# Optimization experiments

Hardware: AMD Instinct MI355X
Metric: run time of the kernel (lower is better)

Reference implementation:

```python
import jax, jax.numpy as jnp
import numpy as np

B, T, H = 4, 8192, 512
LN_EPS = 1e-5


def _ln(x, g, b):
    mu = jnp.mean(x, axis=-1, keepdims=True)
    var = jnp.mean((x - mu) ** 2, axis=-1, keepdims=True)
    return (x - mu) * jax.lax.rsqrt(var + LN_EPS) * g + b


def _log_g(x):
    # log of g(x) = x + 0.5 (x >= 0) else sigmoid(x); both branches NaN-safe.
    return jnp.where(x >= 0, jnp.log(jax.nn.relu(x) + 0.5), -jax.nn.softplus(-x))


def _min_gru(x, Wz, bz, Wh, bh):
    # minGRU parallel log-space scan ("Were RNNs All We Needed?" Alg.), h_0 = 0.
    k = x @ Wz + bz                      # [B,T,H] gate pre-activation
    log_z = -jax.nn.softplus(-k)         # log sigmoid(k)
    log_coeffs = -jax.nn.softplus(k)     # log (1 - sigmoid(k))
    log_tilde_h = _log_g(x @ Wh + bh)
    log_h0 = jnp.full((x.shape[0], 1, x.shape[2]), jnp.log(0.5), x.dtype)  # g(0)=0.5
    log_values = jnp.concatenate([log_h0, log_z + log_tilde_h], axis=1)   # [B,T+1,H]
    a_star = jnp.cumsum(jnp.pad(log_coeffs, ((0, 0), (1, 0), (0, 0))), axis=1)
    log_h = a_star + jax.lax.cumlogsumexp(log_values - a_star, axis=1)
    return jnp.exp(log_h)[:, 1:]         # drop h_0 slot -> [B,T,H]


def setup_inputs() -> dict:
    key = jax.random.key(0)
    ks = jax.random.split(key, 5)
    s = 1.0 / np.sqrt(H)
    return {
        "x": jax.random.normal(ks[0], (B, T, H), jnp.float32),
        "ln1_g": jnp.ones((H,), jnp.float32),
        "ln1_b": jnp.zeros((H,), jnp.float32),
        "Wz": jax.random.normal(ks[1], (H, H), jnp.float32) * s,
        "bz": jnp.zeros((H,), jnp.float32),
        "Wh": jax.random.normal(ks[2], (H, H), jnp.float32) * s,
        "bh": jnp.zeros((H,), jnp.float32),
        "ln2_g": jnp.ones((H,), jnp.float32),
        "ln2_b": jnp.zeros((H,), jnp.float32),
        "W1": jax.random.normal(ks[3], (H, H), jnp.float32) * s,
        "b1": jnp.zeros((H,), jnp.float32),
        "W2": jax.random.normal(ks[4], (H, H), jnp.float32) * s,
        "b2": jnp.zeros((H,), jnp.float32),
    }


def reference(x, ln1_g, ln1_b, Wz, bz, Wh, bh, ln2_g, ln2_b, W1, b1, W2, b2):
    # x = x + minGRU(ln_1(x))   (dropout=0 -> identity)
    x = x + _min_gru(_ln(x, ln1_g, ln1_b), Wz, bz, Wh, bh)
    # x = x + FFN(ln_2(x)) ; FFN = Linear -> ReLU -> Linear (hidden->hidden)
    h = jax.nn.relu(_ln(x, ln2_g, ln2_b) @ W1 + b1)
    x = x + (h @ W2 + b2)
    return x
```

## Files before the change

kernel.cpp:

```cpp
#include <hip/hip_runtime.h>

typedef unsigned short u16;
typedef unsigned int u32;
typedef __bf16 bf16x8 __attribute__((ext_vector_type(8)));
typedef float f32x4 __attribute__((ext_vector_type(4)));
typedef u16 u16x8 __attribute__((ext_vector_type(8)));

__device__ __forceinline__ u16 f2bf(float f) {
    union { float f; u32 i; } v; v.f = f;
    u32 x = v.i;
    u32 r = (x + 0x7fffu + ((x >> 16) & 1u)) >> 16;
    return (u16)r;
}
__device__ __forceinline__ float bf2f(u16 u) {
    union { u32 i; float f; } v; v.i = ((u32)u) << 16; return v.f;
}
__device__ __forceinline__ u16 f2h(float f) {
    union { _Float16 h; u16 u; } v; v.h = (_Float16)f; return v.u;
}
__device__ __forceinline__ float h2f(u16 u) {
    union { _Float16 h; u16 u; } v; v.u = u; return (float)v.h;
}

__device__ __forceinline__ void gld16(const void* g, void* l) {
    __builtin_amdgcn_global_load_lds(
        (const __attribute__((address_space(1))) void*)g,
        (__attribute__((address_space(3))) void*)l, 16, 0, 0);
}

__global__ __launch_bounds__(256) void transpose4(
    const float* __restrict__ s0, const float* __restrict__ s1,
    const float* __restrict__ s2, const float* __restrict__ s3,
    u16* __restrict__ d0, u16* __restrict__ d1,
    u16* __restrict__ d2, u16* __restrict__ d3)
{
    int bx = blockIdx.x;
    int mat = bx >> 8;
    int tile = bx & 255;
    int tx = (tile & 15) * 32;
    int ty = (tile >> 4) * 32;
    const float* src = (mat == 0) ? s0 : (mat == 1) ? s1 : (mat == 2) ? s2 : s3;
    u16* dst = (mat == 0) ? d0 : (mat == 1) ? d1 : (mat == 2) ? d2 : d3;

    __shared__ u16 tl[32][33];
    int col = threadIdx.x & 31;
    int r8  = threadIdx.x >> 5;
    #pragma unroll
    for (int k = 0; k < 4; ++k) {
        int rr = r8 + k * 8;
        tl[rr][col] = f2bf(src[(ty + rr) * 512 + tx + col]);
    }
    __syncthreads();
    #pragma unroll
    for (int k = 0; k < 4; ++k) {
        int rr = r8 + k * 8;
        dst[(tx + rr) * 512 + ty + col] = tl[col][rr];
    }
}

__global__ __launch_bounds__(256) void ln_k(
    const float* __restrict__ x, const float* __restrict__ g,
    const float* __restrict__ b, u16* __restrict__ y, int rows)
{
    int gid = blockIdx.x * blockDim.x + threadIdx.x;
    int row = gid >> 6;
    int lane = gid & 63;
    if (row >= rows) return;

    const float* xr = x + (size_t)row * 512 + lane * 8;
    float4 a0 = *(const float4*)xr;
    float4 a1 = *(const float4*)(xr + 4);
    float f[8] = {a0.x, a0.y, a0.z, a0.w, a1.x, a1.y, a1.z, a1.w};
    float s = 0.f, s2 = 0.f;
    #pragma unroll
    for (int e = 0; e < 8; ++e) { s += f[e]; s2 += f[e] * f[e]; }
    #pragma unroll
    for (int o = 32; o > 0; o >>= 1) { s += __shfl_xor(s, o); s2 += __shfl_xor(s2, o); }
    const float inv = 1.0f / 512.0f;
    float mean = s * inv;
    float var  = s2 * inv - mean * mean;
    float rstd = rsqrtf(var + 1e-5f);

    float4 g0 = *(const float4*)(g + lane * 8);
    float4 g1 = *(const float4*)(g + lane * 8 + 4);
    float4 b0 = *(const float4*)(b + lane * 8);
    float4 b1 = *(const float4*)(b + lane * 8 + 4);
    float gg[8] = {g0.x, g0.y, g0.z, g0.w, g1.x, g1.y, g1.z, g1.w};
    float bb[8] = {b0.x, b0.y, b0.z, b0.w, b1.x, b1.y, b1.z, b1.w};
    u16x8 ov;
    #pragma unroll
    for (int e = 0; e < 8; ++e)
        ov[e] = f2bf((f[e] - mean) * rstd * gg[e] + bb[e]);
    *(u16x8*)(y + (size_t)row * 512 + lane * 8) = ov;
}

template <int MODE>
__global__ __launch_bounds__(256, 2) void gemm_bt(
    const u16* __restrict__ A, const u16* __restrict__ Bt0,
    const u16* __restrict__ Bt1, const float* __restrict__ bias0,
    const float* __restrict__ bias1, const float* __restrict__ resid,
    void* __restrict__ out0v, u16* __restrict__ out1,
    float* __restrict__ chCp, float* __restrict__ chVp)
{
    constexpr int Kd = 512, Nd = 512;
    constexpr int SMEM_N = (MODE == 0) ? 34816 : 8192;
    __shared__ __align__(16) u16 smem[SMEM_N];
    u16* As  = smem;
    u16* Bs0 = smem + 4096;
    u16* Bs1 = smem + 8192;

    int bx = blockIdx.x;
    bx = (bx & 7) * 128 + (bx >> 3);
    int m0 = (bx >> 2) * 128;
    int n0 = (bx & 3) * 128;
    int tid = threadIdx.x;
    int lane = tid & 63;
    int w = tid >> 6;
    int wm = w & 1, wn = w >> 1;
    int l16 = lane & 15;
    int quad = lane >> 4;

    f32x4 acc0[4][4] = {};
    f32x4 acc1[4][4] = {};

    int ch0 = tid, ch1 = tid + 256;
    int row0 = ch0 >> 2, row1 = ch1 >> 2;
    int g0 = (ch0 & 3) ^ ((ch0 >> 3) & 3);
    int g1 = (ch1 & 3) ^ ((ch1 >> 3) & 3);
    const u16* a0p  = A   + (size_t)(m0 + row0) * Kd + g0 * 8;
    const u16* a1p  = A   + (size_t)(m0 + row1) * Kd + g1 * 8;
    const u16* b00p = Bt0 + (size_t)(n0 + row0) * Kd + g0 * 8;
    const u16* b01p = Bt0 + (size_t)(n0 + row1) * Kd + g1 * 8;
    const u16* b10p = (MODE == 0) ? Bt1 + (size_t)(n0 + row0) * Kd + g0 * 8 : nullptr;
    const u16* b11p = (MODE == 0) ? Bt1 + (size_t)(n0 + row1) * Kd + g1 * 8 : nullptr;

    for (int kt = 0; kt < Kd / 32; ++kt) {
        int k0 = kt * 32;
        gld16(a0p  + k0, &As [ch0 * 8]);
        gld16(a1p  + k0, &As [ch1 * 8]);
        gld16(b00p + k0, &Bs0[ch0 * 8]);
        gld16(b01p + k0, &Bs0[ch1 * 8]);
        if (MODE == 0) {
            gld16(b10p + k0, &Bs1[ch0 * 8]);
            gld16(b11p + k0, &Bs1[ch1 * 8]);
        }
        __syncthreads();

        bf16x8 af[4], bf0[4], bf1[4];
        #pragma unroll
        for (int i = 0; i < 4; ++i) {
            int ra = wm * 64 + i * 16 + l16;
            int rb = wn * 64 + i * 16 + l16;
            int ga = quad ^ ((ra >> 1) & 3);
            int gb = quad ^ ((rb >> 1) & 3);
            af[i]  = *(const bf16x8*)&As [ra * 32 + ga * 8];
            bf0[i] = *(const bf16x8*)&Bs0[rb * 32 + gb * 8];
            if (MODE == 0)
                bf1[i] = *(const bf16x8*)&Bs1[rb * 32 + gb * 8];
        }
        #pragma unroll
        for (int i = 0; i < 4; ++i)
            #pragma unroll
            for (int j = 0; j < 4; ++j) {
                acc0[i][j] = __builtin_amdgcn_mfma_f32_16x16x32_bf16(af[i], bf0[j], acc0[i][j], 0, 0, 0);
                if (MODE == 0)
                    acc1[i][j] = __builtin_amdgcn_mfma_f32_16x16x32_bf16(af[i], bf1[j], acc1[i][j], 0, 0, 0);
            }
        __syncthreads();
    }

    if (MODE == 0) {
        u16* Cc = smem;
        u16* Cv = smem + 17408;
        #pragma unroll
        for (int j = 0; j < 4; ++j) {
            int col = n0 + wn * 64 + j * 16 + l16;
            float bk = bias0[col];
            float bhv = bias1[col];
            #pragma unroll
            for (int i = 0; i < 4; ++i)
                #pragma unroll
                for (int r = 0; r < 4; ++r) {
                    int lr = wm * 64 + i * 16 + quad * 4 + r;
                    int lc = wn * 64 + j * 16 + l16;
                    float kk = acc0[i][j][r] + bk;
                    float hh = acc1[i][j][r] + bhv;
                    float z = 1.f / (1.f + __expf(-kk));
                    float c = 1.f / (1.f + __expf(kk));
                    float gg = (hh >= 0.f) ? (hh + 0.5f) : 1.f / (1.f + __expf(-hh));
                    Cc[lr * 136 + lc] = f2h(c);
                    Cv[lr * 136 + lc] = f2h(z * gg);
                }
        }
        __syncthreads();
        u16* cb = (u16*)out0v;
        #pragma unroll
        for (int k = 0; k < 8; ++k) {
            int c = tid + k * 256;
            int row = c >> 4, c8 = c & 15;
            size_t off = (size_t)(m0 + row) * Nd + n0 + c8 * 8;
            *(u16x8*)(cb   + off) = *(const u16x8*)&Cc[row * 136 + c8 * 8];
            *(u16x8*)(out1 + off) = *(const u16x8*)&Cv[row * 136 + c8 * 8];
        }
        int h2 = tid & 127;
        #pragma unroll
        for (int u = 0; u < 2; ++u) {
            int cc = (tid >> 7) + u * 2;
            float C = 1.f, V = 0.f;
            #pragma unroll 8
            for (int t = 0; t < 32; ++t) {
                int lr = cc * 32 + t;
                float c = h2f(Cc[lr * 136 + h2]);
                float v = h2f(Cv[lr * 136 + h2]);
                C *= c;
                V = fmaf(c, V, v);
            }
            int g_row = m0 + cc * 32;
            int b = g_row >> 13;
            int chgl = (g_row & 8191) >> 5;
            int idx = chgl * 2048 + b * 512 + n0 + h2;
            chCp[idx] = C;
            chVp[idx] = V;
        }
    } else {
        #pragma unroll
        for (int j = 0; j < 4; ++j) {
            int col = n0 + wn * 64 + j * 16 + l16;
            float b0 = bias0[col];
            #pragma unroll
            for (int i = 0; i < 4; ++i) {
                #pragma unroll
                for (int r = 0; r < 4; ++r) {
                    int row = m0 + wm * 64 + i * 16 + quad * 4 + r;
                    size_t off = (size_t)row * Nd + col;
                    float v0 = acc0[i][j][r] + b0;
                    if (MODE == 1) {
                        ((u16*)out0v)[off] = f2bf(fmaxf(v0, 0.f));
                    } else {
                        ((float*)out0v)[off] = v0 + resid[off];
                    }
                }
            }
        }
    }
}


__global__ __launch_bounds__(256) void scanB1(
    const float* __restrict__ chC, const float* __restrict__ chV,
    float* __restrict__ scC, float* __restrict__ scV)
{
    int gid = blockIdx.x * 256 + threadIdx.x;
    int s = gid & 2047;
    int sc = gid >> 11;
    float C = 1.f, V = 0.f;
    #pragma unroll 4
    for (int i = 0; i < 16; ++i) {
        int ch = sc * 16 + i;
        float c = chC[ch * 2048 + s];
        float v = chV[ch * 2048 + s];
        C *= c;
        V = fmaf(c, V, v);
    }
    scC[sc * 2048 + s] = C;
    scV[sc * 2048 + s] = V;
}

__global__ __launch_bounds__(256) void scanB2(
    const float* __restrict__ scC, const float* __restrict__ scV,
    float* __restrict__ sst)
{
    int s = blockIdx.x * 256 + threadIdx.x;
    float hcur = 0.5f;
    #pragma unroll
    for (int sc = 0; sc < 16; ++sc) {
        sst[sc * 2048 + s] = hcur;
        hcur = fmaf(scC[sc * 2048 + s], hcur, scV[sc * 2048 + s]);
    }
}

__global__ __launch_bounds__(256) void scanB3(
    const float* __restrict__ chC, const float* __restrict__ chV,
    const float* __restrict__ sst, float* __restrict__ hst)
{
    int gid = blockIdx.x * 256 + threadIdx.x;
    int s = gid & 2047;
    int sc = gid >> 11;
    float hcur = sst[sc * 2048 + s];
    #pragma unroll 4
    for (int i = 0; i < 16; ++i) {
        int ch = sc * 16 + i;
        hst[ch * 2048 + s] = hcur;
        hcur = fmaf(chC[ch * 2048 + s], hcur, chV[ch * 2048 + s]);
    }
}

__global__ __launch_bounds__(256) void scanC(
    const u16* __restrict__ cb, const u16* __restrict__ vb,
    const float* __restrict__ hst, const float* __restrict__ x,
    float* __restrict__ x2)
{
    int gid = blockIdx.x * 256 + threadIdx.x;
    int h = gid & 511;
    int rest = gid >> 9;
    int b = rest & 3;
    int ch = rest >> 2;
    size_t base = ((size_t)(b * 8192 + ch * 32)) * 512 + h;
    float hcur = hst[ch * 2048 + b * 512 + h];
    #pragma unroll 8
    for (int t = 0; t < 32; ++t) {
        size_t off = base + (size_t)t * 512;
        float c = h2f(cb[off]);
        float v = h2f(vb[off]);
        hcur = fmaf(c, hcur, v);
        x2[off] = x[off] + hcur;
    }
}

extern "C" void kernel_launch(void* const* d_in, const int* in_sizes, int n_in,
                              void* d_out, int out_size, void* d_ws, size_t ws_size,
                              hipStream_t stream)
{
    const float* x    = (const float*)d_in[0];
    const float* ln1g = (const float*)d_in[1];
    const float* ln1b = (const float*)d_in[2];
    const float* Wz   = (const float*)d_in[3];
    const float* bz   = (const float*)d_in[4];
    const float* Wh   = (const float*)d_in[5];
    const float* bh   = (const float*)d_in[6];
    const float* ln2g = (const float*)d_in[7];
    const float* ln2b = (const float*)d_in[8];
    const float* W1   = (const float*)d_in[9];
    const float* b1   = (const float*)d_in[10];
    const float* W2   = (const float*)d_in[11];
    const float* b2   = (const float*)d_in[12];
    float* out = (float*)d_out;

    char* ws = (char*)d_ws;
    constexpr size_t MB = 1024 * 1024;
    u16* Wzt = (u16*)(ws);
    u16* Wht = Wzt + 262144;
    u16* W1t = Wzt + 524288;
    u16* W2t = Wzt + 786432;
    u16* a  = (u16*)(ws + 3 * MB + 512 * 1024);
    u16* cb = (u16*)(ws + 35 * MB + 512 * 1024);
    u16* vb = (u16*)(ws + 67 * MB + 512 * 1024);
    float* hst = (float*)(ws + 3 * MB + 512 * 1024);
    float* scC = hst + 524288;
    float* scV = scC + 32768;
    float* sst = scV + 32768;
    float* chC = (float*)d_out;
    float* chV = chC + 524288;

    transpose4<<<1024, 256, 0, stream>>>(Wz, Wh, W1, W2, Wzt, Wht, W1t, W2t);
    ln_k<<<8192, 256, 0, stream>>>(x, ln1g, ln1b, a, 32768);
    gemm_bt<0><<<1024, 256, 0, stream>>>(a, Wzt, Wht, bz, bh, nullptr, cb, vb, chC, chV);
    scanB1<<<128, 256, 0, stream>>>(chC, chV, scC, scV);
    scanB2<<<8, 256, 0, stream>>>(scC, scV, sst);
    scanB3<<<128, 256, 0, stream>>>(chC, chV, sst, hst);
    scanC<<<2048, 256, 0, stream>>>(cb, vb, hst, x, out);
    ln_k<<<8192, 256, 0, stream>>>(out, ln2g, ln2b, a, 32768);
    gemm_bt<1><<<1024, 256, 0, stream>>>(a, W1t, nullptr, b1, nullptr, nullptr, cb, nullptr, nullptr, nullptr);
    gemm_bt<2><<<1024, 256, 0, stream>>>(cb, W2t, nullptr, b2, nullptr, out, out, nullptr, nullptr, nullptr);
}
```

Measured before the change: 314.0 us.

## Compute chunk scan summaries in registers via shuffles, drop LDS staging

The MODE 0 GEMM epilogue no longer stages the gate and value tiles in a large shared-memory buffer. Each lane now reduces its own accumulator rows and combines partial (C,V) pairs across quads with xor-shuffles to form 32-row chunk summaries. It also writes the fp16 outputs directly from registers and derives c as 1-z with fast reciprocals. Shared memory drops from about 68KB to 24KB, which should allow more resident blocks and removes a barrier. The cost is scattered 2-byte global stores instead of coalesced 16-byte ones, and slightly different rounding from computing c as 1-z.

Result: faster. 304.0 us (-3.2%).

```diff
diff --git a/kernel.cpp b/kernel.cpp
--- a/kernel.cpp
+++ b/kernel.cpp
@@ -103,7 +103,7 @@
     float* __restrict__ chCp, float* __restrict__ chVp)
 {
     constexpr int Kd = 512, Nd = 512;
-    constexpr int SMEM_N = (MODE == 0) ? 34816 : 8192;
+    constexpr int SMEM_N = (MODE == 0) ? 12288 : 8192;
     __shared__ __align__(16) u16 smem[SMEM_N];
     u16* As  = smem;
     u16* Bs0 = smem + 4096;
@@ -170,57 +170,59 @@
     }
 
     if (MODE == 0) {
-        u16* Cc = smem;
-        u16* Cv = smem + 17408;
-        #pragma unroll
-        for (int j = 0; j < 4; ++j) {
-            int col = n0 + wn * 64 + j * 16 + l16;
-            float bk = bias0[col];
-            float bhv = bias1[col];
-            #pragma unroll
-            for (int i = 0; i < 4; ++i)
-                #pragma unroll
-                for (int r = 0; r < 4; ++r) {
-                    int lr = wm * 64 + i * 16 + quad * 4 + r;
-                    int lc = wn * 64 + j * 16 + l16;
-                    float kk = acc0[i][j][r] + bk;
-                    float hh = acc1[i][j][r] + bhv;
-                    float z = 1.f / (1.f + __expf(-kk));
-                    float c = 1.f / (1.f + __expf(kk));
-                    float gg = (hh >= 0.f) ? (hh + 0.5f) : 1.f / (1.f + __expf(-hh));
-                    Cc[lr * 136 + lc] = f2h(c);
-                    Cv[lr * 136 + lc] = f2h(z * gg);
-                }
-        }
-        __syncthreads();
         u16* cb = (u16*)out0v;
         #pragma unroll
-        for (int k = 0; k < 8; ++k) {
-            int c = tid + k * 256;
-            int row = c >> 4, c8 = c & 15;
-            size_t off = (size_t)(m0 + row) * Nd + n0 + c8 * 8;
-            *(u16x8*)(cb   + off) = *(const u16x8*)&Cc[row * 136 + c8 * 8];
-            *(u16x8*)(out1 + off) = *(const u16x8*)&Cv[row * 136 + c8 * 8];
-        }
-        int h2 = tid & 127;
-        #pragma unroll
-        for (int u = 0; u < 2; ++u) {
-            int cc = (tid >> 7) + u * 2;
-            float C = 1.f, V = 0.f;
-            #pragma unroll 8
-            for (int t = 0; t < 32; ++t) {
-                int lr = cc * 32 + t;
-                float c = h2f(Cc[lr * 136 + h2]);
-                float v = h2f(Cv[lr * 136 + h2]);
-                C *= c;
-                V = fmaf(c, V, v);
+        for (int p = 0; p < 2; ++p) {
+            int grow = m0 + wm * 64 + p * 32;
+            int bb_  = grow >> 13;
+            int chgl = (grow & 8191) >> 5;
+            #pragma unroll
+            for (int j = 0; j < 4; ++j) {
+                int col = n0 + wn * 64 + j * 16 + l16;
+                float bk  = bias0[col];
+                float bh2 = bias1[col];
+                float Cs[2], Vs[2];
+                #pragma unroll
+                for (int ii = 0; ii < 2; ++ii) {
+                    int i = 2 * p + ii;
+                    float C = 1.f, V = 0.f;
+                    #pragma unroll
+                    for (int r = 0; r < 4; ++r) {
+                        int row = m0 + wm * 64 + i * 16 + quad * 4 + r;
+                        float kk = acc0[i][j][r] + bk;
+                        float hh = acc1[i][j][r] + bh2;
+                        float z = __builtin_amdgcn_rcpf(1.f + __expf(-kk));
+                        float c = 1.f - z;
+                        float gs = __builtin_amdgcn_rcpf(1.f + __expf(-hh));
+                        float gg = (hh >= 0.f) ? (hh + 0.5f) : gs;
+                        float v = z * gg;
+                        size_t off = (size_t)row * Nd + col;
+                        cb[off]   = f2h(c);
+                        out1[off] = f2h(v);
+                        C *= c;
+                        V = fmaf(c, V, v);
+                    }
+                    Cs[ii] = C; Vs[ii] = V;
+                }
+                #pragma unroll
+                for (int ii = 0; ii < 2; ++ii) {
+                    float C = Cs[ii], V = Vs[ii];
+                    float oc = __shfl_xor(C, 16), ov = __shfl_xor(V, 16);
+                    V = (quad & 1) ? fmaf(C, ov, V) : fmaf(oc, V, ov);
+                    C *= oc;
+                    oc = __shfl_xor(C, 32); ov = __shfl_xor(V, 32);
+                    V = (quad & 2) ? fmaf(C, ov, V) : fmaf(oc, V, ov);
+                    C *= oc;
+                    Cs[ii] = C; Vs[ii] = V;
+                }
+                float Cch = Cs[0] * Cs[1];
+                float Vch = fmaf(Cs[1], Vs[0], Vs[1]);
+                if (quad == 0) {
+                    int idx = chgl * 2048 + bb_ * 512 + col;
+                    chCp[idx] = Cch;
+                    chVp[idx] = Vch;
+                }
             }
-            int g_row = m0 + cc * 32;
-            int b = g_row >> 13;
-            int chgl = (g_row & 8191) >> 5;
-            int idx = chgl * 2048 + b * 512 + n0 + h2;
-            chCp[idx] = C;
-            chVp[idx] = V;
         }
     } else {
         #pragma unroll
```
